# Kernel tuning notes

Hardware: AMD Instinct MI355X
Metric: run time of the kernel (lower is better)

The kernel has to match this reference:

```python
import jax, jax.numpy as jnp
import numpy as np

KERNEL = 3  # unfold kernel size (stride 1, no padding)

def _unfold(x, k):
    # torch.nn.Unfold(kernel_size=k) equivalent: (B, C, H, W) -> (B, C*k*k, L)
    # channel ordering: index = c*k*k + i*k + j (channel outermost), matching torch.
    B, C, H, W = x.shape
    Ho, Wo = H - k + 1, W - k + 1
    cols = [x[:, :, i:i + Ho, j:j + Wo] for i in range(k) for j in range(k)]  # k*k x (B,C,Ho,Wo)
    u = jnp.stack(cols, axis=2)  # (B, C, k*k, Ho, Wo)
    return u.reshape(B, C * k * k, Ho * Wo)


def setup_inputs() -> dict:
    key = jax.random.key(0)
    k1, k2, k3, k4 = jax.random.split(key, 4)
    B, C, H, W = 512, 3, 64, 64
    M = 512            # num_neurons
    K = C * KERNEL * KERNEL   # input_dim = 27
    L = (H - KERNEL + 1) * (W - KERNEL + 1)  # 3844 patches
    O = 10             # output_dim
    x = jax.random.normal(k1, (B, C, H, W), dtype=jnp.float32)
    G = jax.random.normal(k2, (M, L), dtype=jnp.float32)
    # original inits v,w to zeros; use randn for a non-degenerate reference
    v = jax.random.normal(k3, (M, K, O), dtype=jnp.float32) * 0.02
    w = jax.random.normal(k4, (M, K, O), dtype=jnp.float32) * 0.02
    return {"x": x, "G": G, "v": v, "w": w}


def reference(x, G, v, w):
    # Faithful to:
    #   U = unfold(x)                         (B, K, L)
    #   t = einsum('mn,ikn->imnk', G, U)      (B, M, L, K)  <- never materialized here
    #   out = einsum('ijkl,jlm->im', t, v-w)  (B, O)
    # Reordered as two small contractions (same math, no huge intermediate):
    U = _unfold(x, KERNEL)                    # (B, K, L)
    A = jnp.einsum('bkn,mn->bmk', U, G)       # (B, M, K): contract over patches L
    p_diff = v - w                            # (M, K, O)
    out = jnp.einsum('bmk,mko->bo', A, p_diff)  # (B, O)
    return out
```

## Files before the change

kernel.cpp:

```cpp
#include <hip/hip_runtime.h>
#include <hip/hip_bf16.h>

#define ODIM   10
#define HOg    62
#define LDIM   3844
#define CHW    12288
#define BATCH  512
#define KO     270
#define KOP    272
#define MDIM   512

typedef __attribute__((ext_vector_type(8))) short bfrag;
typedef __attribute__((ext_vector_type(4))) float f32x4;

__global__ __launch_bounds__(256)
void prep_kernel(const float* __restrict__ G,
                 const float* __restrict__ v, const float* __restrict__ w,
                 __hip_bfloat16* __restrict__ Gt,
                 __hip_bfloat16* __restrict__ Pdt,
                 float* __restrict__ out) {
    const int b = blockIdx.x;
    if (b < 488) {
        __shared__ float tile[64][65];
        const int nTile = b % 61;
        const int mTile = b / 61;
        const int n0 = nTile * 64;
        const int m0 = mTile * 64;
        const int tc = threadIdx.x & 63;
        const int tr = threadIdx.x >> 6;
#pragma unroll
        for (int rr = 0; rr < 64; rr += 4) {
            int n = n0 + tc;
            tile[rr + tr][tc] = (n < LDIM) ? G[(size_t)(m0 + rr + tr) * LDIM + n] : 0.f;
        }
        __syncthreads();
        const int nr = threadIdx.x >> 2;
        const int ms = (threadIdx.x & 3) * 16;
        __hip_bfloat16 buf[16];
#pragma unroll
        for (int i = 0; i < 16; ++i)
            buf[i] = __float2bfloat16(tile[ms + i][nr]);
        __hip_bfloat16* dst = Gt + (size_t)(n0 + nr) * MDIM + m0 + ms;
        *reinterpret_cast<uint4*>(dst)     = *reinterpret_cast<uint4*>(&buf[0]);
        *reinterpret_cast<uint4*>(dst + 8) = *reinterpret_cast<uint4*>(&buf[8]);
    } else if (b < 1032) {
        int idx = (b - 488) * 256 + threadIdx.x;
        int m  = idx / KOP;
        int ko = idx - m * KOP;
        float val = (ko < KO) ? (v[m * KO + ko] - w[m * KO + ko]) : 0.f;
        Pdt[(size_t)ko * MDIM + m] = __float2bfloat16(val);
    } else {
        int idx = (b - 1032) * 256 + threadIdx.x;
        out[idx] = 0.f;
    }
}

__global__ __launch_bounds__(256, 4)
void tmfma_kernel(const __hip_bfloat16* __restrict__ Pdt,
                  const __hip_bfloat16* __restrict__ Gt,
                  float* __restrict__ T) {
    const int orig = blockIdx.x;
    const int xcd  = orig & 7;
    const int base = orig >> 3;
    const int lb   = (xcd < 5 ? xcd * 130 : 650 + (xcd - 5) * 129) + base;
    const int kt   = lb % 17;
    const int tile = lb / 17;

    const int wv   = threadIdx.x >> 6;
    const int lane = threadIdx.x & 63;
    const int n0   = tile * 64;
    const int ko0  = kt * 16;
    const int row  = lane & 15;
    const int kg   = lane >> 4;

    const __hip_bfloat16* Ap = Pdt + (size_t)(ko0 + row) * MDIM + wv * 128 + kg * 8;
    const __hip_bfloat16* Bp = Gt  + (size_t)(n0 + row) * MDIM + wv * 128 + kg * 8;

    f32x4 acc[4];
#pragma unroll
    for (int j = 0; j < 4; ++j) acc[j] = (f32x4){0.f, 0.f, 0.f, 0.f};

#pragma unroll
    for (int ks = 0; ks < 4; ++ks) {
        bfrag a = *reinterpret_cast<const bfrag*>(Ap + ks * 32);
#pragma unroll
        for (int j = 0; j < 4; ++j) {
            bfrag bfr = *reinterpret_cast<const bfrag*>(
                Bp + (size_t)j * 16 * MDIM + ks * 32);
            acc[j] = __builtin_amdgcn_mfma_f32_16x16x32_bf16(a, bfr, acc[j], 0, 0, 0);
        }
    }

    __shared__ f32x4 redL[3][64][4];
    if (wv > 0) {
#pragma unroll
        for (int j = 0; j < 4; ++j) redL[wv - 1][lane][j] = acc[j];
    }
    __syncthreads();
    if (wv == 0) {
#pragma unroll
        for (int j = 0; j < 4; ++j) {
            acc[j] += redL[0][lane][j];
            acc[j] += redL[1][lane][j];
            acc[j] += redL[2][lane][j];
        }
#pragma unroll
        for (int j = 0; j < 4; ++j) {
            int col = n0 + j * 16 + row;
            if (col < LDIM) {
#pragma unroll
                for (int r = 0; r < 4; ++r) {
                    int ro = ko0 + kg * 4 + r;
                    if (ro < KO)
                        T[(size_t)ro * LDIM + col] = acc[j][r];
                }
            }
        }
    }
}

__global__ __launch_bounds__(256)
void fold_kernel(const float* __restrict__ T, float* __restrict__ S) {
    int idx = blockIdx.x * 256 + threadIdx.x;
    if (idx >= ODIM * CHW) return;
    int o   = idx / CHW;
    int chw = idx - o * CHW;
    int c = chw >> 12;
    int h = (chw >> 6) & 63;
    int w = chw & 63;

    float s = 0.f;
    for (int i = 0; i < 3; ++i) {
        int pi = h - i;
        if ((unsigned)pi >= HOg) continue;
        for (int j = 0; j < 3; ++j) {
            int pj = w - j;
            if ((unsigned)pj >= HOg) continue;
            int ko = (c * 9 + i * 3 + j) * ODIM + o;
            s += T[(size_t)ko * LDIM + pi * HOg + pj];
        }
    }
    S[idx] = s;
}

__global__ __launch_bounds__(256)
void out_gemm_kernel(const float* __restrict__ X,
                     const float* __restrict__ S,
                     float* __restrict__ out) {
    const int bg = blockIdx.x / 6;
    const int sl = blockIdx.x % 6;
    const int b0 = bg * 8;
    const int i0 = sl * 512;
    const int tid = threadIdx.x;
    const int NV = CHW / 4;

    const float4* X4 = reinterpret_cast<const float4*>(X);
    const float4* S4 = reinterpret_cast<const float4*>(S);

    float acc[8][ODIM];
#pragma unroll
    for (int im = 0; im < 8; ++im)
#pragma unroll
        for (int o = 0; o < ODIM; ++o) acc[im][o] = 0.f;

#pragma unroll
    for (int ii = 0; ii < 2; ++ii) {
        int i = i0 + tid + ii * 256;
        float4 xv[8];
#pragma unroll
        for (int im = 0; im < 8; ++im)
            xv[im] = X4[(size_t)(b0 + im) * NV + i];
#pragma unroll
        for (int o = 0; o < ODIM; ++o) {
            float4 sv = S4[(size_t)o * NV + i];
#pragma unroll
            for (int im = 0; im < 8; ++im) {
                acc[im][o] += xv[im].x * sv.x + xv[im].y * sv.y
                            + xv[im].z * sv.z + xv[im].w * sv.w;
            }
        }
    }

#pragma unroll
    for (int im = 0; im < 8; ++im)
#pragma unroll
        for (int o = 0; o < ODIM; ++o) {
            float s = acc[im][o];
            for (int off = 32; off > 0; off >>= 1)
                s += __shfl_down(s, off, 64);
            acc[im][o] = s;
        }

    __shared__ float red[4][80];
    const int wave = tid >> 6;
    const int lane = tid & 63;
    if (lane == 0) {
#pragma unroll
        for (int im = 0; im < 8; ++im)
#pragma unroll
            for (int o = 0; o < ODIM; ++o)
                red[wave][im * ODIM + o] = acc[im][o];
    }
    __syncthreads();
    if (tid < 80) {
        float t = red[0][tid] + red[1][tid] + red[2][tid] + red[3][tid];
        int im = tid / ODIM;
        int o  = tid - im * ODIM;
        atomicAdd(&out[(size_t)(b0 + im) * ODIM + o], t);
    }
}

extern "C" void kernel_launch(void* const* d_in, const int* in_sizes, int n_in,
                              void* d_out, int out_size, void* d_ws, size_t ws_size,
                              hipStream_t stream) {
    const float* x = (const float*)d_in[0];
    const float* G = (const float*)d_in[1];
    const float* v = (const float*)d_in[2];
    const float* w = (const float*)d_in[3];
    float* out = (float*)d_out;

    char* wsb = (char*)d_ws;
    float*          T   = (float*)wsb;
    __hip_bfloat16* Gt  = (__hip_bfloat16*)(wsb + 4151520);
    __hip_bfloat16* Pdt = (__hip_bfloat16*)(wsb + 4151520 + 3997696);
    float*          S   = (float*)(wsb + 4151520 + 3997696 + 278528);

    prep_kernel<<<1052, 256, 0, stream>>>(G, v, w, Gt, Pdt, out);

    tmfma_kernel<<<1037, 256, 0, stream>>>(Pdt, Gt, T);

    fold_kernel<<<(ODIM * CHW + 255) / 256, 256, 0, stream>>>(T, S);

    out_gemm_kernel<<<384, 256, 0, stream>>>(x, S, out);
}
```

Before: 46.30 us.

## Retile MFMA GEMM with LDS double-buffering and larger tiles, split out_gemm finer

The T GEMM kernel moves from 16x64 tiles with a cross-wave split-K reduction to 32x128 tiles. Operands are staged through double-buffered LDS and the kernel iterates over the full K=512 in 8 steps, which cuts redundant global loads of Gt and Pdt and removes the LDS reduction. Gt and Pdt are padded (NPAD 3968, KOP2 288) so loads stay in bounds, and Pdt is now written coalesced. out_gemm uses twice as many blocks, each doing half the work, for more parallelism. The catch is only 279 GEMM blocks, so occupancy is lower.

```diff
diff --git a/kernel.cpp b/kernel.cpp
--- a/kernel.cpp
+++ b/kernel.cpp
@@ -7,8 +7,10 @@
 #define CHW    12288
 #define BATCH  512
 #define KO     270
-#define KOP    272
+#define KOP2   288
 #define MDIM   512
+#define NPAD   3968
+#define LROW   72
 
 typedef __attribute__((ext_vector_type(8))) short bfrag;
 typedef __attribute__((ext_vector_type(4))) float f32x4;
@@ -20,10 +22,10 @@
                  __hip_bfloat16* __restrict__ Pdt,
                  float* __restrict__ out) {
     const int b = blockIdx.x;
-    if (b < 488) {
+    if (b < 496) {
         __shared__ float tile[64][65];
-        const int nTile = b % 61;
-        const int mTile = b / 61;
+        const int nTile = b % 62;
+        const int mTile = b / 62;
         const int n0 = nTile * 64;
         const int m0 = mTile * 64;
         const int tc = threadIdx.x & 63;
@@ -43,76 +45,127 @@
         __hip_bfloat16* dst = Gt + (size_t)(n0 + nr) * MDIM + m0 + ms;
         *reinterpret_cast<uint4*>(dst)     = *reinterpret_cast<uint4*>(&buf[0]);
         *reinterpret_cast<uint4*>(dst + 8) = *reinterpret_cast<uint4*>(&buf[8]);
-    } else if (b < 1032) {
-        int idx = (b - 488) * 256 + threadIdx.x;
-        int m  = idx / KOP;
-        int ko = idx - m * KOP;
+    } else if (b < 1072) {
+        int idx = (b - 496) * 256 + threadIdx.x;
+        int ko = idx >> 9;
+        int m  = idx & 511;
         float val = (ko < KO) ? (v[m * KO + ko] - w[m * KO + ko]) : 0.f;
-        Pdt[(size_t)ko * MDIM + m] = __float2bfloat16(val);
+        Pdt[idx] = __float2bfloat16(val);
     } else {
-        int idx = (b - 1032) * 256 + threadIdx.x;
+        int idx = (b - 1072) * 256 + threadIdx.x;
         out[idx] = 0.f;
     }
 }
 
-__global__ __launch_bounds__(256, 4)
+__global__ __launch_bounds__(256, 2)
 void tmfma_kernel(const __hip_bfloat16* __restrict__ Pdt,
                   const __hip_bfloat16* __restrict__ Gt,
                   float* __restrict__ T) {
     const int orig = blockIdx.x;
     const int xcd  = orig & 7;
-    const int base = orig >> 3;
-    const int lb   = (xcd < 5 ? xcd * 130 : 650 + (xcd - 5) * 129) + base;
-    const int kt   = lb % 17;
-    const int tile = lb / 17;
-
-    const int wv   = threadIdx.x >> 6;
-    const int lane = threadIdx.x & 63;
-    const int n0   = tile * 64;
-    const int ko0  = kt * 16;
-    const int row  = lane & 15;
+    const int q8   = orig >> 3;
+    const int lb   = (xcd < 7 ? xcd * 35 : 245) + (xcd < 7 ? q8 : q8);
+    const int lbf  = (xcd < 7 ? xcd * 35 + q8 : 245 + q8);
+    const int kt   = lbf % 9;
+    const int nt   = lbf / 9;
+    (void)lb;
+    const int ko0  = kt * 32;
+    const int n0   = nt * 128;
+
+    const int tid  = threadIdx.x;
+    const int wv   = tid >> 6;
+    const int lane = tid & 63;
+    const int r16  = lane & 15;
     const int kg   = lane >> 4;
 
-    const __hip_bfloat16* Ap = Pdt + (size_t)(ko0 + row) * MDIM + wv * 128 + kg * 8;
-    const __hip_bfloat16* Bp = Gt  + (size_t)(n0 + row) * MDIM + wv * 128 + kg * 8;
-
-    f32x4 acc[4];
-#pragma unroll
-    for (int j = 0; j < 4; ++j) acc[j] = (f32x4){0.f, 0.f, 0.f, 0.f};
-
-#pragma unroll
-    for (int ks = 0; ks < 4; ++ks) {
-        bfrag a = *reinterpret_cast<const bfrag*>(Ap + ks * 32);
-#pragma unroll
-        for (int j = 0; j < 4; ++j) {
-            bfrag bfr = *reinterpret_cast<const bfrag*>(
-                Bp + (size_t)j * 16 * MDIM + ks * 32);
-            acc[j] = __builtin_amdgcn_mfma_f32_16x16x32_bf16(a, bfr, acc[j], 0, 0, 0);
-        }
-    }
-
-    __shared__ f32x4 redL[3][64][4];
-    if (wv > 0) {
-#pragma unroll
-        for (int j = 0; j < 4; ++j) redL[wv - 1][lane][j] = acc[j];
-    }
+    __shared__ __hip_bfloat16 ldsA[2][32 * LROW];
+    __shared__ __hip_bfloat16 ldsB[2][128 * LROW];
+
+    const int srow  = tid >> 3;
+    const int slot  = tid & 7;
+    const __hip_bfloat16* pA = Pdt + (size_t)(ko0 + srow) * MDIM + slot * 8;
+    const __hip_bfloat16* pB0 = Gt + (size_t)(n0 +       srow) * MDIM + slot * 8;
+    const __hip_bfloat16* pB1 = Gt + (size_t)(n0 +  32 + srow) * MDIM + slot * 8;
+    const __hip_bfloat16* pB2 = Gt + (size_t)(n0 +  64 + srow) * MDIM + slot * 8;
+    const __hip_bfloat16* pB3 = Gt + (size_t)(n0 +  96 + srow) * MDIM + slot * 8;
+    const int aoff  = srow * LROW + slot * 8;
+    const int boff0 = (      srow) * LROW + slot * 8;
+    const int boff1 = ( 32 + srow) * LROW + slot * 8;
+    const int boff2 = ( 64 + srow) * LROW + slot * 8;
+    const int boff3 = ( 96 + srow) * LROW + slot * 8;
+
+    f32x4 acc00 = {0.f,0.f,0.f,0.f}, acc01 = {0.f,0.f,0.f,0.f};
+    f32x4 acc10 = {0.f,0.f,0.f,0.f}, acc11 = {0.f,0.f,0.f,0.f};
+
+    uint4 rA, rB0, rB1, rB2, rB3;
+
+#define LDREGS(t)                                                         \
+    do { int k0 = (t) * 64;                                               \
+        rA  = *reinterpret_cast<const uint4*>(pA  + k0);                  \
+        rB0 = *reinterpret_cast<const uint4*>(pB0 + k0);                  \
+        rB1 = *reinterpret_cast<const uint4*>(pB1 + k0);                  \
+        rB2 = *reinterpret_cast<const uint4*>(pB2 + k0);                  \
+        rB3 = *reinterpret_cast<const uint4*>(pB3 + k0);                  \
+    } while (0)
+
+#define WRLDS(bsel)                                                       \
+    do {                                                                  \
+        *reinterpret_cast<uint4*>(&ldsA[bsel][aoff])  = rA;               \
+        *reinterpret_cast<uint4*>(&ldsB[bsel][boff0]) = rB0;              \
+        *reinterpret_cast<uint4*>(&ldsB[bsel][boff1]) = rB1;              \
+        *reinterpret_cast<uint4*>(&ldsB[bsel][boff2]) = rB2;              \
+        *reinterpret_cast<uint4*>(&ldsB[bsel][boff3]) = rB3;              \
+    } while (0)
+
+#define COMPUTE(bsel)                                                     \
+    do {                                                                  \
+        _Pragma("unroll")                                                 \
+        for (int ks = 0; ks < 2; ++ks) {                                  \
+            int kb = ks * 32 + kg * 8;                                    \
+            bfrag a0 = *reinterpret_cast<const bfrag*>(                   \
+                &ldsA[bsel][(r16) * LROW + kb]);                          \
+            bfrag a1 = *reinterpret_cast<const bfrag*>(                   \
+                &ldsA[bsel][(16 + r16) * LROW + kb]);                     \
+            bfrag b0 = *reinterpret_cast<const bfrag*>(                   \
+                &ldsB[bsel][(wv * 32 + r16) * LROW + kb]);                \
+            bfrag b1 = *reinterpret_cast<const bfrag*>(                   \
+                &ldsB[bsel][(wv * 32 + 16 + r16) * LROW + kb]);           \
+            acc00 = __builtin_amdgcn_mfma_f32_16x16x32_bf16(a0, b0, acc00, 0, 0, 0); \
+            acc01 = __builtin_amdgcn_mfma_f32_16x16x32_bf16(a0, b1, acc01, 0, 0, 0); \
+            acc10 = __builtin_amdgcn_mfma_f32_16x16x32_bf16(a1, b0, acc10, 0, 0, 0); \
+            acc11 = __builtin_amdgcn_mfma_f32_16x16x32_bf16(a1, b1, acc11, 0, 0, 0); \
+        }                                                                 \
+    } while (0)
+
+    LDREGS(0);
+    WRLDS(0);
     __syncthreads();
-    if (wv == 0) {
-#pragma unroll
-        for (int j = 0; j < 4; ++j) {
-            acc[j] += redL[0][lane][j];
-            acc[j] += redL[1][lane][j];
-            acc[j] += redL[2][lane][j];
-        }
-#pragma unroll
-        for (int j = 0; j < 4; ++j) {
-            int col = n0 + j * 16 + row;
+
+#pragma unroll
+    for (int t = 0; t < 8; ++t) {
+        const int cur = t & 1;
+        if (t < 7) LDREGS(t + 1);
+        COMPUTE(cur);
+        if (t < 7) WRLDS(cur ^ 1);
+        __syncthreads();
+    }
+#undef LDREGS
+#undef WRLDS
+#undef COMPUTE
+
+    const f32x4* accs[4] = { &acc00, &acc01, &acc10, &acc11 };
+#pragma unroll
+    for (int f = 0; f < 2; ++f) {
+#pragma unroll
+        for (int g = 0; g < 2; ++g) {
+            const f32x4 a = *accs[f * 2 + g];
+            int col = n0 + wv * 32 + g * 16 + r16;
             if (col < LDIM) {
 #pragma unroll
                 for (int r = 0; r < 4; ++r) {
-                    int ro = ko0 + kg * 4 + r;
+                    int ro = ko0 + f * 16 + kg * 4 + r;
                     if (ro < KO)
-                        T[(size_t)ro * LDIM + col] = acc[j][r];
+                        T[(size_t)ro * LDIM + col] = a[r];
                 }
             }
         }
@@ -147,12 +200,12 @@
 void out_gemm_kernel(const float* __restrict__ X,
                      const float* __restrict__ S,
                      float* __restrict__ out) {
-    const int bg = blockIdx.x / 6;
-    const int sl = blockIdx.x % 6;
+    const int bg = blockIdx.x / 12;
+    const int sl = blockIdx.x % 12;
     const int b0 = bg * 8;
-    const int i0 = sl * 512;
     const int tid = threadIdx.x;
     const int NV = CHW / 4;
+    const int i  = sl * 256 + tid;
 
     const float4* X4 = reinterpret_cast<const float4*>(X);
     const float4* S4 = reinterpret_cast<const float4*>(S);
@@ -163,21 +216,17 @@
 #pragma unroll
         for (int o = 0; o < ODIM; ++o) acc[im][o] = 0.f;
 
-#pragma unroll
-    for (int ii = 0; ii < 2; ++ii) {
-        int i = i0 + tid + ii * 256;
-        float4 xv[8];
-#pragma unroll
-        for (int im = 0; im < 8; ++im)
-            xv[im] = X4[(size_t)(b0 + im) * NV + i];
-#pragma unroll
-        for (int o = 0; o < ODIM; ++o) {
-            float4 sv = S4[(size_t)o * NV + i];
-#pragma unroll
-            for (int im = 0; im < 8; ++im) {
-                acc[im][o] += xv[im].x * sv.x + xv[im].y * sv.y
-                            + xv[im].z * sv.z + xv[im].w * sv.w;
-            }
+    float4 xv[8];
+#pragma unroll
+    for (int im = 0; im < 8; ++im)
+        xv[im] = X4[(size_t)(b0 + im) * NV + i];
+#pragma unroll
+    for (int o = 0; o < ODIM; ++o) {
+        float4 sv = S4[(size_t)o * NV + i];
+#pragma unroll
+        for (int im = 0; im < 8; ++im) {
+            acc[im][o] += xv[im].x * sv.x + xv[im].y * sv.y
+                        + xv[im].z * sv.z + xv[im].w * sv.w;
         }
     }
 
@@ -222,14 +271,14 @@
     char* wsb = (char*)d_ws;
     float*          T   = (float*)wsb;
     __hip_bfloat16* Gt  = (__hip_bfloat16*)(wsb + 4151520);
-    __hip_bfloat16* Pdt = (__hip_bfloat16*)(wsb + 4151520 + 3997696);
-    float*          S   = (float*)(wsb + 4151520 + 3997696 + 278528);
-
-    prep_kernel<<<1052, 256, 0, stream>>>(G, v, w, Gt, Pdt, out);
-
-    tmfma_kernel<<<1037, 256, 0, stream>>>(Pdt, Gt, T);
+    __hip_bfloat16* Pdt = (__hip_bfloat16*)(wsb + 4151520 + 4063232);
+    float*          S   = (float*)(wsb + 4151520 + 4063232 + 294912);
+
+    prep_kernel<<<1092, 256, 0, stream>>>(G, v, w, Gt, Pdt, out);
+
+    tmfma_kernel<<<279, 256, 0, stream>>>(Pdt, Gt, T);
 
     fold_kernel<<<(ODIM * CHW + 255) / 256, 256, 0, stream>>>(T, S);
 
-    out_gemm_kernel<<<384, 256, 0, stream>>>(x, S, out);
-}
+    out_gemm_kernel<<<768, 256, 0, stream>>>(x, S, out);
+}
```

Result: faster. 45.38 us (-2.0%).
